# Kernel tuning notes

Measured on AMD Instinct MI355X. Metric: run time of the kernel, lower is better.

## Reference

```python
import jax, jax.numpy as jnp
import numpy as np

DIM = 1024
NUM_HEADS = 16
NUM_KV_HEADS = 4
HEAD_DIM = DIM // NUM_HEADS  # 64
QK_GAIN = 1.5
ROPE_BASE = 10000.0


def _rms_norm(x, eps):
    # F.rms_norm with no weight: x / sqrt(mean(x^2) + eps)
    ms = jnp.mean(jnp.square(x), axis=-1, keepdims=True)
    return x * jax.lax.rsqrt(ms + eps)


def _rope_tables(seqlen, dim, dtype):
    inv_freq = 1.0 / (ROPE_BASE ** (jnp.arange(0, dim, 2, dtype=jnp.float32) / dim))
    freqs = jnp.outer(jnp.arange(seqlen, dtype=jnp.float32), inv_freq)  # [N, D/2]
    emb = jnp.concatenate([freqs, freqs], axis=-1)  # [N, D]
    return jnp.cos(emb).astype(dtype), jnp.sin(emb).astype(dtype)


def _apply_rope(x, cos, sin):
    # x: [B, N, H, D]; cos/sin: [N, D] broadcast over batch and heads
    half = x.shape[-1] // 2
    rot = jnp.concatenate([-x[..., half:], x[..., :half]], axis=-1)
    return x * cos[None, :, None, :] + rot * sin[None, :, None, :]


def setup_inputs() -> dict:
    key = jax.random.key(0)
    ks = jax.random.split(key, 5)
    B, N, C = 4, 2048, DIM
    s = 0.02
    return {
        "x": jax.random.normal(ks[0], (B, N, C), dtype=jnp.float32),
        "wq": jax.random.normal(ks[1], (C, C), dtype=jnp.float32) * s,
        "wk": jax.random.normal(ks[2], (C, NUM_KV_HEADS * HEAD_DIM), dtype=jnp.float32) * s,
        "wv": jax.random.normal(ks[3], (C, NUM_KV_HEADS * HEAD_DIM), dtype=jnp.float32) * s,
        "wo": jax.random.normal(ks[4], (C, C), dtype=jnp.float32) * s,
    }


def reference(x, wq, wk, wv, wo) -> jnp.ndarray:
    B, N, C = x.shape
    H, Hkv, D = NUM_HEADS, NUM_KV_HEADS, HEAD_DIM
    eps = jnp.finfo(x.dtype).eps

    q = (x @ wq).reshape(B, N, H, D)
    k = (x @ wk).reshape(B, N, Hkv, D)
    v = (x @ wv).reshape(B, N, Hkv, D)

    q = _rms_norm(q, eps)
    k = _rms_norm(k, eps)

    cos, sin = _rope_tables(N, D, q.dtype)
    q = _apply_rope(q, cos, sin) * QK_GAIN
    k = _apply_rope(k, cos, sin)

    # GQA head expansion (repeat_interleave along head dim)
    g = H // Hkv
    k = jnp.repeat(k, g, axis=2)  # [B, N, H, D]
    v = jnp.repeat(v, g, axis=2)

    # causal SDPA, scale = 1/sqrt(D)
    scores = jnp.einsum("bqhd,bkhd->bhqk", q, k) / jnp.sqrt(jnp.asarray(D, q.dtype))
    causal = jnp.tril(jnp.ones((N, N), dtype=bool))
    scores = jnp.where(causal[None, None], scores, jnp.finfo(scores.dtype).min)
    probs = jax.nn.softmax(scores, axis=-1)
    y = jnp.einsum("bhqk,bkhd->bqhd", probs, v).reshape(B, N, C)
    return y @ wo
```

## Files before the change

kernel.cpp:

```cpp
#include <hip/hip_runtime.h>

typedef __bf16 bf16;
typedef __bf16 bf16x8 __attribute__((ext_vector_type(8)));
typedef __bf16 bf16x4 __attribute__((ext_vector_type(4)));
typedef float f32x4 __attribute__((ext_vector_type(4)));

#define B_ 4
#define N_ 2048
#define C_ 1024
#define H_ 16
#define HKV_ 4
#define D_ 64

#define QSCALE 0.2705053201666806f
#define NEGINF (-1.0e30f)

__device__ int g_ctr;

__global__ __launch_bounds__(256) void prep_qkv(const float* __restrict__ wq,
                                                const float* __restrict__ wk,
                                                const float* __restrict__ wv,
                                                bf16* __restrict__ wT) {
  __shared__ __align__(16) bf16 lds[64 * 72];
  int bx = blockIdx.x;
  const float* w;
  int ncols, tk, tn, nbase;
  if (bx < 256) {
    w = wq; ncols = 1024; tk = bx >> 4; tn = bx & 15; nbase = 0;
  } else if (bx < 320) {
    int t = bx - 256;
    w = wk; ncols = 256; tk = t >> 2; tn = t & 3; nbase = 1024;
  } else {
    int t = bx - 320;
    w = wv; ncols = 256; tk = t >> 2; tn = t & 3; nbase = 1280;
  }
  int tid = threadIdx.x;
#pragma unroll
  for (int i = 0; i < 4; ++i) {
    int c = tid + i * 256;
    int kr = c >> 4, n4 = (c & 15) * 4;
    f32x4 v = *(const f32x4*)(w + (size_t)(tk * 64 + kr) * ncols + tn * 64 + n4);
    bf16x4 b;
#pragma unroll
    for (int j = 0; j < 4; ++j) b[j] = (bf16)v[j];
    *(bf16x4*)(lds + kr * 72 + n4) = b;
  }
  __syncthreads();
#pragma unroll
  for (int i = 0; i < 2; ++i) {
    int c = tid + i * 256;
    int n = c >> 3, koff = (c & 7) * 8;
    bf16x8 tv;
#pragma unroll
    for (int j = 0; j < 8; ++j) tv[j] = lds[(koff + j) * 72 + n];
    *(bf16x8*)(wT + (size_t)(nbase + tn * 64 + n) * 1024 + tk * 64 + koff) = tv;
  }
}

__global__ __launch_bounds__(256) void prep_wo(const float* __restrict__ w,
                                               bf16* __restrict__ wT) {
  __shared__ __align__(16) bf16 lds[64 * 72];
  int tk = blockIdx.x >> 4, tn = blockIdx.x & 15;
  int tid = threadIdx.x;
#pragma unroll
  for (int i = 0; i < 4; ++i) {
    int c = tid + i * 256;
    int kr = c >> 4, n4 = (c & 15) * 4;
    f32x4 v = *(const f32x4*)(w + (size_t)(tk * 64 + kr) * 1024 + tn * 64 + n4);
    bf16x4 b;
#pragma unroll
    for (int j = 0; j < 4; ++j) b[j] = (bf16)v[j];
    *(bf16x4*)(lds + kr * 72 + n4) = b;
  }
  __syncthreads();
#pragma unroll
  for (int i = 0; i < 2; ++i) {
    int c = tid + i * 256;
    int n = c >> 3, koff = (c & 7) * 8;
    bf16x8 tv;
#pragma unroll
    for (int j = 0; j < 8; ++j) tv[j] = lds[(koff + j) * 72 + n];
    *(bf16x8*)(wT + (size_t)(tn * 64 + n) * 1024 + tk * 64 + koff) = tv;
  }
}

__global__ __launch_bounds__(256) void gemm_qkv(const float* __restrict__ x,
                                                const bf16* __restrict__ wT,
                                                bf16* __restrict__ qb,
                                                bf16* __restrict__ kvb) {
  __shared__ __align__(16) bf16 As[128 * 72];
  __shared__ __align__(16) bf16 Bs[128 * 72];
  int by = blockIdx.y;
  int n0 = by * 128;
  bf16* Out;
  int ostride, ocol0;
  if (by < 8) {
    Out = qb; ostride = 1024; ocol0 = by * 128;
  } else if (by < 10) {
    Out = kvb; ostride = 512; ocol0 = (by - 8) * 128;
  } else {
    Out = kvb; ostride = 512; ocol0 = 256 + (by - 10) * 128;
  }
  int m0 = blockIdx.x * 128;
  int tid = threadIdx.x;
  int wave = tid >> 6, lane = tid & 63;
  int quad = lane >> 4, lr = lane & 15;
  int wr = (wave >> 1) * 64, wc = (wave & 1) * 64;

  f32x4 acc[4][4];
  const f32x4 z = {0.f, 0.f, 0.f, 0.f};
#pragma unroll
  for (int i = 0; i < 4; ++i)
#pragma unroll
    for (int j = 0; j < 4; ++j) acc[i][j] = z;

  for (int k0 = 0; k0 < 1024; k0 += 64) {
    __syncthreads();
#pragma unroll
    for (int i = 0; i < 8; ++i) {
      int c = tid + i * 256;
      int row = c >> 4, off4 = (c & 15) * 4;
      f32x4 av = *(const f32x4*)(x + (size_t)(m0 + row) * 1024 + k0 + off4);
      bf16x4 a16;
#pragma unroll
      for (int j = 0; j < 4; ++j) a16[j] = (bf16)av[j];
      *(bf16x4*)(As + row * 72 + off4) = a16;
    }
#pragma unroll
    for (int i = 0; i < 4; ++i) {
      int c = tid + i * 256;
      int row = c >> 3, off = (c & 7) * 8;
      *(bf16x8*)(Bs + row * 72 + off) =
          *(const bf16x8*)(wT + (size_t)(n0 + row) * 1024 + k0 + off);
    }
    __syncthreads();
#pragma unroll
    for (int kx = 0; kx < 2; ++kx) {
      bf16x8 af[4], bfr[4];
#pragma unroll
      for (int t = 0; t < 4; ++t) {
        af[t] = *(const bf16x8*)(As + (wr + t * 16 + lr) * 72 + kx * 32 + quad * 8);
        bfr[t] = *(const bf16x8*)(Bs + (wc + t * 16 + lr) * 72 + kx * 32 + quad * 8);
      }
#pragma unroll
      for (int rt = 0; rt < 4; ++rt)
#pragma unroll
        for (int ct = 0; ct < 4; ++ct)
          acc[rt][ct] = __builtin_amdgcn_mfma_f32_16x16x32_bf16(af[rt], bfr[ct],
                                                                acc[rt][ct], 0, 0, 0);
    }
  }
#pragma unroll
  for (int rt = 0; rt < 4; ++rt)
#pragma unroll
    for (int ct = 0; ct < 4; ++ct)
#pragma unroll
      for (int r = 0; r < 4; ++r) {
        int row = m0 + wr + rt * 16 + quad * 4 + r;
        int col = ocol0 + wc + ct * 16 + lr;
        Out[(size_t)row * ostride + col] = (bf16)acc[rt][ct][r];
      }
}

__global__ __launch_bounds__(256) void gemm_out(const bf16* __restrict__ A,
                                                const bf16* __restrict__ Bt,
                                                float* __restrict__ C) {
  __shared__ __align__(16) bf16 As[128 * 72];
  __shared__ __align__(16) bf16 Bs[128 * 72];
  int m0 = blockIdx.x * 128, n0 = blockIdx.y * 128;
  int tid = threadIdx.x;
  int wave = tid >> 6, lane = tid & 63;
  int quad = lane >> 4, lr = lane & 15;
  int wr = (wave >> 1) * 64, wc = (wave & 1) * 64;

  f32x4 acc[4][4];
  const f32x4 z = {0.f, 0.f, 0.f, 0.f};
#pragma unroll
  for (int i = 0; i < 4; ++i)
#pragma unroll
    for (int j = 0; j < 4; ++j) acc[i][j] = z;

  for (int k0 = 0; k0 < 1024; k0 += 64) {
    __syncthreads();
#pragma unroll
    for (int i = 0; i < 4; ++i) {
      int c = tid + i * 256;
      int row = c >> 3, off = (c & 7) * 8;
      *(bf16x8*)(As + row * 72 + off) =
          *(const bf16x8*)(A + (size_t)(m0 + row) * 1024 + k0 + off);
      *(bf16x8*)(Bs + row * 72 + off) =
          *(const bf16x8*)(Bt + (size_t)(n0 + row) * 1024 + k0 + off);
    }
    __syncthreads();
#pragma unroll
    for (int kx = 0; kx < 2; ++kx) {
      bf16x8 af[4], bfr[4];
#pragma unroll
      for (int t = 0; t < 4; ++t) {
        af[t] = *(const bf16x8*)(As + (wr + t * 16 + lr) * 72 + kx * 32 + quad * 8);
        bfr[t] = *(const bf16x8*)(Bs + (wc + t * 16 + lr) * 72 + kx * 32 + quad * 8);
      }
#pragma unroll
      for (int rt = 0; rt < 4; ++rt)
#pragma unroll
        for (int ct = 0; ct < 4; ++ct)
          acc[rt][ct] = __builtin_amdgcn_mfma_f32_16x16x32_bf16(af[rt], bfr[ct],
                                                                acc[rt][ct], 0, 0, 0);
    }
  }
#pragma unroll
  for (int rt = 0; rt < 4; ++rt)
#pragma unroll
    for (int ct = 0; ct < 4; ++ct)
#pragma unroll
      for (int r = 0; r < 4; ++r) {
        int row = m0 + wr + rt * 16 + quad * 4 + r;
        int col = n0 + wc + ct * 16 + lr;
        C[(size_t)row * 1024 + col] = acc[rt][ct][r];
      }
}

__global__ __launch_bounds__(256) void transpose_v(const bf16* __restrict__ kv,
                                                   bf16* __restrict__ vt) {
  __shared__ __align__(16) bf16 lds[64 * 72];
  if (blockIdx.x == 0 && blockIdx.y == 0 && threadIdx.x == 0) g_ctr = 0;
  int nt = blockIdx.x;
  int bh = blockIdx.y;
  int b = bh >> 2, hkv = bh & 3;
  int tid = threadIdx.x;
#pragma unroll
  for (int i = 0; i < 2; ++i) {
    int c = tid + i * 256;
    int tok = c >> 3, off = (c & 7) * 8;
    *(bf16x8*)(lds + tok * 72 + off) =
        *(const bf16x8*)(kv + (size_t)(b * N_ + nt * 64 + tok) * 512 + 256 + hkv * 64 + off);
  }
  __syncthreads();
#pragma unroll
  for (int i = 0; i < 2; ++i) {
    int c = tid + i * 256;
    int d = c >> 3, toff = (c & 7) * 8;
    bf16x8 tv;
#pragma unroll
    for (int j = 0; j < 8; ++j) tv[j] = lds[(toff + j) * 72 + d];
    *(bf16x8*)(vt + ((size_t)bh * 64 + d) * N_ + nt * 64 + toff) = tv;
  }
}

__global__ __launch_bounds__(256) void norm_rope(bf16* __restrict__ q,
                                                 bf16* __restrict__ kv) {
  int wave = threadIdx.x >> 6, lane = threadIdx.x & 63;
  int hid = blockIdx.x * 4 + wave;
  int t = hid / 20;
  int sub = hid - t * 20;
  int n = t & (N_ - 1);
  bf16* ptr;
  float oscale;
  if (sub < 16) {
    ptr = q + ((size_t)t * 16 + sub) * 64;
    oscale = QSCALE;
  } else {
    ptr = kv + (size_t)t * 512 + (sub - 16) * 64;
    oscale = 1.0f;
  }
  float x = (float)ptr[lane];
  float ss = x * x;
  ss += __shfl_xor(ss, 1);
  ss += __shfl_xor(ss, 2);
  ss += __shfl_xor(ss, 4);
  ss += __shfl_xor(ss, 8);
  ss += __shfl_xor(ss, 16);
  ss += __shfl_xor(ss, 32);
  float rn = rsqrtf(ss * (1.0f / 64.0f) + 1.1920929e-07f);
  float xn = x * rn;
  float pr = __shfl_xor(xn, 32);
  float rot = (lane < 32) ? -pr : pr;
  float ang = (float)n * exp2f(-0.41524101186092029f * (float)(lane & 31));
  float sv, cv;
  __sincosf(ang, &sv, &cv);
  ptr[lane] = (bf16)((xn * cv + rot * sv) * oscale);
}

__global__ __launch_bounds__(256) void attn(bf16* __restrict__ q,
                                            const bf16* __restrict__ kv,
                                            const bf16* __restrict__ vt) {
  __shared__ __align__(16) bf16 Ks[64 * 64];
  __shared__ __align__(16) bf16 Vs[64 * 64];
  __shared__ __align__(16) bf16 Ps[64 * 64];
  __shared__ int s_item;
  int tid = threadIdx.x;
  int wave = tid >> 6, lane = tid & 63;
  int quad = lane >> 4, lr = lane & 15;
  int srow = tid >> 3, soff = (tid & 7) * 8;
  int su = ((tid & 7) ^ (srow & 7)) * 8;
  int e7 = lr & 7;
  const f32x4 z = {0.f, 0.f, 0.f, 0.f};

  while (true) {
    if (tid == 0) s_item = atomicAdd(&g_ctr, 1);
    __syncthreads();
    int item = s_item;
    if (item >= 2048) break;
    int j = 31 - (item >> 6);
    int rr = item & 63;
    int b = rr & 3, h = rr >> 2, hkv = h >> 2;
    int qrow0 = j * 64 + wave * 16;
    int nkt = j + 1;

    bf16x8 qf[2];
#pragma unroll
    for (int kx = 0; kx < 2; ++kx)
      qf[kx] = *(const bf16x8*)(
          q + ((size_t)(b * N_ + qrow0 + lr) * H_ + h) * D_ + kx * 32 + quad * 8);

    f32x4 acc[4];
    float m_i = NEGINF, l_i = 0.f;
#pragma unroll
    for (int dt = 0; dt < 4; ++dt) acc[dt] = z;

    const bf16* kp = kv + (size_t)(b * N_ + srow) * 512 + hkv * 64 + soff;
    const bf16* vp = vt + ((size_t)(b * HKV_ + hkv) * 64 + srow) * N_ + soff;

    bf16x8 sk0, sk1, sv0, sv1;
    sk0 = *(const bf16x8*)(kp);
    sk1 = *(const bf16x8*)(kp + 32 * 512);
    sv0 = *(const bf16x8*)(vp);
    sv1 = *(const bf16x8*)(vp + 32 * N_);
    *(bf16x8*)(Ks + srow * 64 + su) = sk0;
    *(bf16x8*)(Ks + (srow + 32) * 64 + su) = sk1;
    *(bf16x8*)(Vs + srow * 64 + su) = sv0;
    *(bf16x8*)(Vs + (srow + 32) * 64 + su) = sv1;
    asm volatile("s_waitcnt lgkmcnt(0)" ::: "memory");
    __builtin_amdgcn_s_barrier();
    __builtin_amdgcn_sched_barrier(0);

    for (int kt = 0; kt < nkt; ++kt) {
      bool pf = (kt + 1 < nkt);
      if (pf) {
        kp += 64 * 512;
        vp += 64;
        sk0 = *(const bf16x8*)(kp);
        sk1 = *(const bf16x8*)(kp + 32 * 512);
        sv0 = *(const bf16x8*)(vp);
        sv1 = *(const bf16x8*)(vp + 32 * N_);
      }

      f32x4 st[4];
#pragma unroll
      for (int ct = 0; ct < 4; ++ct) st[ct] = z;
#pragma unroll
      for (int kx = 0; kx < 2; ++kx) {
        bf16x8 kf[4];
#pragma unroll
        for (int ct = 0; ct < 4; ++ct)
          kf[ct] = *(const bf16x8*)(Ks + (ct * 16 + lr) * 64 + (((kx * 4 + quad) ^ e7) * 8));
        __builtin_amdgcn_s_setprio(1);
#pragma unroll
        for (int ct = 0; ct < 4; ++ct)
          st[ct] = __builtin_amdgcn_mfma_f32_16x16x32_bf16(kf[ct], qf[kx], st[ct], 0, 0, 0);
        __builtin_amdgcn_s_setprio(0);
      }
      if (kt == j) {
        int qrow = qrow0 + lr;
#pragma unroll
        for (int ct = 0; ct < 4; ++ct)
#pragma unroll
          for (int r = 0; r < 4; ++r) {
            int key = kt * 64 + ct * 16 + quad * 4 + r;
            if (key > qrow) st[ct][r] = NEGINF;
          }
      }
      float mx = NEGINF;
#pragma unroll
      for (int ct = 0; ct < 4; ++ct)
#pragma unroll
        for (int r = 0; r < 4; ++r) mx = fmaxf(mx, st[ct][r]);
      mx = fmaxf(mx, __shfl_xor(mx, 16));
      mx = fmaxf(mx, __shfl_xor(mx, 32));
      if (__any(mx > m_i + 8.0f)) {
        float mnew = fmaxf(m_i, mx);
        float alpha = exp2f(m_i - mnew);
        m_i = mnew;
        l_i *= alpha;
#pragma unroll
        for (int dt = 0; dt < 4; ++dt)
#pragma unroll
          for (int r = 0; r < 4; ++r) acc[dt][r] *= alpha;
      }
      float rs = 0.f;
#pragma unroll
      for (int ct = 0; ct < 4; ++ct)
#pragma unroll
        for (int r = 0; r < 4; ++r) {
          float p = exp2f(st[ct][r] - m_i);
          st[ct][r] = p;
          rs += p;
        }
      rs += __shfl_xor(rs, 16);
      rs += __shfl_xor(rs, 32);
      l_i += rs;
#pragma unroll
      for (int ct = 0; ct < 4; ++ct) {
        bf16x4 pk;
#pragma unroll
        for (int r = 0; r < 4; ++r) pk[r] = (bf16)st[ct][r];
        int pu = (((ct * 2) + (quad >> 1)) ^ e7) * 8 + (quad & 1) * 4;
        *(bf16x4*)(Ps + (wave * 16 + lr) * 64 + pu) = pk;
      }
      asm volatile("s_waitcnt lgkmcnt(0)" ::: "memory");
#pragma unroll
      for (int kx = 0; kx < 2; ++kx) {
        bf16x8 vf[4], pfr;
#pragma unroll
        for (int dt = 0; dt < 4; ++dt)
          vf[dt] = *(const bf16x8*)(Vs + (dt * 16 + lr) * 64 + (((kx * 4 + quad) ^ e7) * 8));
        pfr = *(const bf16x8*)(Ps + (wave * 16 + lr) * 64 + (((kx * 4 + quad) ^ e7) * 8));
        __builtin_amdgcn_s_setprio(1);
#pragma unroll
        for (int dt = 0; dt < 4; ++dt)
          acc[dt] = __builtin_amdgcn_mfma_f32_16x16x32_bf16(vf[dt], pfr, acc[dt], 0, 0, 0);
        __builtin_amdgcn_s_setprio(0);
      }

      __builtin_amdgcn_s_barrier();
      __builtin_amdgcn_sched_barrier(0);
      if (pf) {
        *(bf16x8*)(Ks + srow * 64 + su) = sk0;
        *(bf16x8*)(Ks + (srow + 32) * 64 + su) = sk1;
        *(bf16x8*)(Vs + srow * 64 + su) = sv0;
        *(bf16x8*)(Vs + (srow + 32) * 64 + su) = sv1;
        asm volatile("s_waitcnt lgkmcnt(0)" ::: "memory");
      }
      __builtin_amdgcn_s_barrier();
      __builtin_amdgcn_sched_barrier(0);
    }

    float inv = 1.0f / l_i;
    int qrow = qrow0 + lr;
#pragma unroll
    for (int dt = 0; dt < 4; ++dt) {
      bf16x4 ov;
#pragma unroll
      for (int r = 0; r < 4; ++r) ov[r] = (bf16)(acc[dt][r] * inv);
      *(bf16x4*)(q + ((size_t)(b * N_ + qrow) * H_ + h) * D_ + dt * 16 + quad * 4) = ov;
    }
  }
}

extern "C" void kernel_launch(void* const* d_in, const int* in_sizes, int n_in,
                              void* d_out, int out_size, void* d_ws, size_t ws_size,
                              hipStream_t stream) {
  const float* x = (const float*)d_in[0];
  const float* wq = (const float*)d_in[1];
  const float* wk = (const float*)d_in[2];
  const float* wv = (const float*)d_in[3];
  const float* wo = (const float*)d_in[4];
  float* out = (float*)d_out;
  char* ws = (char*)d_ws;
  bf16* q = (bf16*)(ws);
  bf16* kv = (bf16*)(ws + 16777216);
  bf16* vt = (bf16*)(ws + 25165824);
  bf16* wqkvT = (bf16*)(ws + 25165824);
  bf16* woT = (bf16*)(ws + 25165824);

  prep_qkv<<<dim3(384), 256, 0, stream>>>(wq, wk, wv, wqkvT);
  gemm_qkv<<<dim3(64, 12), 256, 0, stream>>>(x, wqkvT, q, kv);
  norm_rope<<<dim3(40960), 256, 0, stream>>>(q, kv);
  transpose_v<<<dim3(32, 16), 256, 0, stream>>>(kv, vt);
  attn<<<dim3(1536), 256, 0, stream>>>(q, kv, vt);
  prep_wo<<<dim3(256), 256, 0, stream>>>(wo, woT);
  gemm_out<<<dim3(64, 8), 256, 0, stream>>>(q, woT, out);
}
```

Before: 288.0 us.

## Register-prefetch GEMM tiles across iterations and vectorize norm_rope to 8 elements per thread

Both projection GEMMs now load the next K-tile from global memory into registers while MFMAs run on the current LDS tile. The data is written to LDS after a barrier, and s_setprio is raised around the MFMA block. This aims to hide global load latency behind compute, at the cost of more registers (the f32 prefetch buffer for x). norm_rope switches from one bf16 per lane to 8-wide vector loads and stores with 8 threads per head, which cuts the shuffle count and the block count.

```diff
diff --git a/kernel.cpp b/kernel.cpp
--- a/kernel.cpp
+++ b/kernel.cpp
@@ -106,6 +106,8 @@
   int wave = tid >> 6, lane = tid & 63;
   int quad = lane >> 4, lr = lane & 15;
   int wr = (wave >> 1) * 64, wc = (wave & 1) * 64;
+  int arow = tid >> 4, aoff = (tid & 15) * 4;
+  int brow = tid >> 3, boff = (tid & 7) * 8;
 
   f32x4 acc[4][4];
   const f32x4 z = {0.f, 0.f, 0.f, 0.f};
@@ -114,26 +116,37 @@
 #pragma unroll
     for (int j = 0; j < 4; ++j) acc[i][j] = z;
 
+  f32x4 sa[8];
+  bf16x8 sb[4];
+#pragma unroll
+  for (int i = 0; i < 8; ++i)
+    sa[i] = *(const f32x4*)(x + (size_t)(m0 + arow + i * 16) * 1024 + aoff);
+#pragma unroll
+  for (int i = 0; i < 4; ++i)
+    sb[i] = *(const bf16x8*)(wT + (size_t)(n0 + brow + i * 32) * 1024 + boff);
+#pragma unroll
+  for (int i = 0; i < 8; ++i) {
+    bf16x4 a16;
+#pragma unroll
+    for (int j = 0; j < 4; ++j) a16[j] = (bf16)sa[i][j];
+    *(bf16x4*)(As + (arow + i * 16) * 72 + aoff) = a16;
+  }
+#pragma unroll
+  for (int i = 0; i < 4; ++i) *(bf16x8*)(Bs + (brow + i * 32) * 72 + boff) = sb[i];
+  asm volatile("s_waitcnt lgkmcnt(0)" ::: "memory");
+  __builtin_amdgcn_s_barrier();
+  __builtin_amdgcn_sched_barrier(0);
+
   for (int k0 = 0; k0 < 1024; k0 += 64) {
-    __syncthreads();
-#pragma unroll
-    for (int i = 0; i < 8; ++i) {
-      int c = tid + i * 256;
-      int row = c >> 4, off4 = (c & 15) * 4;
-      f32x4 av = *(const f32x4*)(x + (size_t)(m0 + row) * 1024 + k0 + off4);
-      bf16x4 a16;
-#pragma unroll
-      for (int j = 0; j < 4; ++j) a16[j] = (bf16)av[j];
-      *(bf16x4*)(As + row * 72 + off4) = a16;
-    }
-#pragma unroll
-    for (int i = 0; i < 4; ++i) {
-      int c = tid + i * 256;
-      int row = c >> 3, off = (c & 7) * 8;
-      *(bf16x8*)(Bs + row * 72 + off) =
-          *(const bf16x8*)(wT + (size_t)(n0 + row) * 1024 + k0 + off);
-    }
-    __syncthreads();
+    bool pf = (k0 + 64 < 1024);
+    if (pf) {
+#pragma unroll
+      for (int i = 0; i < 8; ++i)
+        sa[i] = *(const f32x4*)(x + (size_t)(m0 + arow + i * 16) * 1024 + k0 + 64 + aoff);
+#pragma unroll
+      for (int i = 0; i < 4; ++i)
+        sb[i] = *(const bf16x8*)(wT + (size_t)(n0 + brow + i * 32) * 1024 + k0 + 64 + boff);
+    }
 #pragma unroll
     for (int kx = 0; kx < 2; ++kx) {
       bf16x8 af[4], bfr[4];
@@ -142,13 +155,31 @@
         af[t] = *(const bf16x8*)(As + (wr + t * 16 + lr) * 72 + kx * 32 + quad * 8);
         bfr[t] = *(const bf16x8*)(Bs + (wc + t * 16 + lr) * 72 + kx * 32 + quad * 8);
       }
+      __builtin_amdgcn_s_setprio(1);
 #pragma unroll
       for (int rt = 0; rt < 4; ++rt)
 #pragma unroll
         for (int ct = 0; ct < 4; ++ct)
           acc[rt][ct] = __builtin_amdgcn_mfma_f32_16x16x32_bf16(af[rt], bfr[ct],
                                                                 acc[rt][ct], 0, 0, 0);
-    }
+      __builtin_amdgcn_s_setprio(0);
+    }
+    __builtin_amdgcn_s_barrier();
+    __builtin_amdgcn_sched_barrier(0);
+    if (pf) {
+#pragma unroll
+      for (int i = 0; i < 8; ++i) {
+        bf16x4 a16;
+#pragma unroll
+        for (int j = 0; j < 4; ++j) a16[j] = (bf16)sa[i][j];
+        *(bf16x4*)(As + (arow + i * 16) * 72 + aoff) = a16;
+      }
+#pragma unroll
+      for (int i = 0; i < 4; ++i) *(bf16x8*)(Bs + (brow + i * 32) * 72 + boff) = sb[i];
+      asm volatile("s_waitcnt lgkmcnt(0)" ::: "memory");
+    }
+    __builtin_amdgcn_s_barrier();
+    __builtin_amdgcn_sched_barrier(0);
   }
 #pragma unroll
   for (int rt = 0; rt < 4; ++rt)
@@ -172,6 +203,7 @@
   int wave = tid >> 6, lane = tid & 63;
   int quad = lane >> 4, lr = lane & 15;
   int wr = (wave >> 1) * 64, wc = (wave & 1) * 64;
+  int brow = tid >> 3, boff = (tid & 7) * 8;
 
   f32x4 acc[4][4];
   const f32x4 z = {0.f, 0.f, 0.f, 0.f};
@@ -180,18 +212,30 @@
 #pragma unroll
     for (int j = 0; j < 4; ++j) acc[i][j] = z;
 
+  bf16x8 sa[4], sb[4];
+#pragma unroll
+  for (int i = 0; i < 4; ++i) {
+    sa[i] = *(const bf16x8*)(A + (size_t)(m0 + brow + i * 32) * 1024 + boff);
+    sb[i] = *(const bf16x8*)(Bt + (size_t)(n0 + brow + i * 32) * 1024 + boff);
+  }
+#pragma unroll
+  for (int i = 0; i < 4; ++i) {
+    *(bf16x8*)(As + (brow + i * 32) * 72 + boff) = sa[i];
+    *(bf16x8*)(Bs + (brow + i * 32) * 72 + boff) = sb[i];
+  }
+  asm volatile("s_waitcnt lgkmcnt(0)" ::: "memory");
+  __builtin_amdgcn_s_barrier();
+  __builtin_amdgcn_sched_barrier(0);
+
   for (int k0 = 0; k0 < 1024; k0 += 64) {
-    __syncthreads();
-#pragma unroll
-    for (int i = 0; i < 4; ++i) {
-      int c = tid + i * 256;
-      int row = c >> 3, off = (c & 7) * 8;
-      *(bf16x8*)(As + row * 72 + off) =
-          *(const bf16x8*)(A + (size_t)(m0 + row) * 1024 + k0 + off);
-      *(bf16x8*)(Bs + row * 72 + off) =
-          *(const bf16x8*)(Bt + (size_t)(n0 + row) * 1024 + k0 + off);
-    }
-    __syncthreads();
+    bool pf = (k0 + 64 < 1024);
+    if (pf) {
+#pragma unroll
+      for (int i = 0; i < 4; ++i) {
+        sa[i] = *(const bf16x8*)(A + (size_t)(m0 + brow + i * 32) * 1024 + k0 + 64 + boff);
+        sb[i] = *(const bf16x8*)(Bt + (size_t)(n0 + brow + i * 32) * 1024 + k0 + 64 + boff);
+      }
+    }
 #pragma unroll
     for (int kx = 0; kx < 2; ++kx) {
       bf16x8 af[4], bfr[4];
@@ -200,13 +244,27 @@
         af[t] = *(const bf16x8*)(As + (wr + t * 16 + lr) * 72 + kx * 32 + quad * 8);
         bfr[t] = *(const bf16x8*)(Bs + (wc + t * 16 + lr) * 72 + kx * 32 + quad * 8);
       }
+      __builtin_amdgcn_s_setprio(1);
 #pragma unroll
       for (int rt = 0; rt < 4; ++rt)
 #pragma unroll
         for (int ct = 0; ct < 4; ++ct)
           acc[rt][ct] = __builtin_amdgcn_mfma_f32_16x16x32_bf16(af[rt], bfr[ct],
                                                                 acc[rt][ct], 0, 0, 0);
-    }
+      __builtin_amdgcn_s_setprio(0);
+    }
+    __builtin_amdgcn_s_barrier();
+    __builtin_amdgcn_sched_barrier(0);
+    if (pf) {
+#pragma unroll
+      for (int i = 0; i < 4; ++i) {
+        *(bf16x8*)(As + (brow + i * 32) * 72 + boff) = sa[i];
+        *(bf16x8*)(Bs + (brow + i * 32) * 72 + boff) = sb[i];
+      }
+      asm volatile("s_waitcnt lgkmcnt(0)" ::: "memory");
+    }
+    __builtin_amdgcn_s_barrier();
+    __builtin_amdgcn_sched_barrier(0);
   }
 #pragma unroll
   for (int rt = 0; rt < 4; ++rt)
@@ -249,36 +307,46 @@
 
 __global__ __launch_bounds__(256) void norm_rope(bf16* __restrict__ q,
                                                  bf16* __restrict__ kv) {
-  int wave = threadIdx.x >> 6, lane = threadIdx.x & 63;
-  int hid = blockIdx.x * 4 + wave;
-  int t = hid / 20;
-  int sub = hid - t * 20;
+  int tid = threadIdx.x;
+  int g = (blockIdx.x << 5) + (tid >> 3);
+  int e = tid & 7;
+  int t = g / 20;
+  int sub = g - t * 20;
   int n = t & (N_ - 1);
   bf16* ptr;
   float oscale;
   if (sub < 16) {
-    ptr = q + ((size_t)t * 16 + sub) * 64;
+    ptr = q + (size_t)t * 1024 + sub * 64;
     oscale = QSCALE;
   } else {
     ptr = kv + (size_t)t * 512 + (sub - 16) * 64;
     oscale = 1.0f;
   }
-  float x = (float)ptr[lane];
-  float ss = x * x;
+  bf16x8 v = *(const bf16x8*)(ptr + e * 8);
+  float xv[8];
+  float ss = 0.f;
+#pragma unroll
+  for (int i = 0; i < 8; ++i) {
+    xv[i] = (float)v[i];
+    ss += xv[i] * xv[i];
+  }
   ss += __shfl_xor(ss, 1);
   ss += __shfl_xor(ss, 2);
   ss += __shfl_xor(ss, 4);
-  ss += __shfl_xor(ss, 8);
-  ss += __shfl_xor(ss, 16);
-  ss += __shfl_xor(ss, 32);
   float rn = rsqrtf(ss * (1.0f / 64.0f) + 1.1920929e-07f);
-  float xn = x * rn;
-  float pr = __shfl_xor(xn, 32);
-  float rot = (lane < 32) ? -pr : pr;
-  float ang = (float)n * exp2f(-0.41524101186092029f * (float)(lane & 31));
-  float sv, cv;
-  __sincosf(ang, &sv, &cv);
-  ptr[lane] = (bf16)((xn * cv + rot * sv) * oscale);
+  float base = (float)((e & 3) * 8);
+  bf16x8 o;
+#pragma unroll
+  for (int i = 0; i < 8; ++i) {
+    float xn = xv[i] * rn;
+    float pr = __shfl_xor(xn, 4);
+    float rot = (e < 4) ? -pr : pr;
+    float ang = (float)n * exp2f(-0.41524101186092029f * (base + (float)i));
+    float sv, cv;
+    __sincosf(ang, &sv, &cv);
+    o[i] = (bf16)((xn * cv + rot * sv) * oscale);
+  }
+  *(bf16x8*)(ptr + e * 8) = o;
 }
 
 __global__ __launch_bounds__(256) void attn(bf16* __restrict__ q,
@@ -465,7 +533,7 @@
 
   prep_qkv<<<dim3(384), 256, 0, stream>>>(wq, wk, wv, wqkvT);
   gemm_qkv<<<dim3(64, 12), 256, 0, stream>>>(x, wqkvT, q, kv);
-  norm_rope<<<dim3(40960), 256, 0, stream>>>(q, kv);
+  norm_rope<<<dim3(5120), 256, 0, stream>>>(q, kv);
   transpose_v<<<dim3(32, 16), 256, 0, stream>>>(kv, vt);
   attn<<<dim3(1536), 256, 0, stream>>>(q, kv, vt);
   prep_wo<<<dim3(256), 256, 0, stream>>>(wo, woT);
```

Result: faster. 265.4 us (-7.9%).
